# Optimization experiments

Measured on AMD Instinct MI355X. Metric: run time of the kernel, lower is better.

## Reference

```python
import jax, jax.numpy as jnp
import numpy as np

D_MODEL = 512
N_HEADS = 8
HEAD_DIM = D_MODEL // N_HEADS  # 64
N_LAYERS = 2
D_FF = 4 * D_MODEL
B, L, INPUT_DIM = 4, 1024, 32
SAMPLE_K = 35  # min(factor*ceil(ln L), L) with factor=5, L=1024
N_CLASSES = 10


def _layernorm(x, g, b, eps=1e-5):
    m = x.mean(-1, keepdims=True)
    v = ((x - m) ** 2).mean(-1, keepdims=True)
    return (x - m) / jnp.sqrt(v + eps) * g + b


def _pos_encoding(length, d):
    pos = np.arange(length, dtype=np.float32)[:, None]
    div = np.exp(np.arange(0, d, 2, dtype=np.float32) * (-np.log(10000.0) / d))
    pe = np.zeros((length, d), np.float32)
    pe[:, 0::2] = np.sin(pos * div)
    pe[:, 1::2] = np.cos(pos * div)
    return jnp.asarray(pe)


def _prob_attention(Q, K, V, idx_sample):
    # Q,K,V: (B,H,L,E); idx_sample: (L, sample_k) int
    b, h, l, e = Q.shape
    n_top = idx_sample.shape[-1]  # u == sample_k here since L_Q == L_K
    # K_sample gather: (B,H,L,sample_k,E)
    Ks = K[:, :, idx_sample, :]
    QK_sample = jnp.einsum('bhie,bhije->bhij', Q, Ks)  # (B,H,L,sample_k)
    M = QK_sample.max(-1) - QK_sample.mean(-1)          # sparsity measure
    _, idx_top = jax.lax.top_k(M, n_top)                # (B,H,n_top)
    Qr = jnp.take_along_axis(Q, idx_top[..., None], axis=2)  # (B,H,n_top,E)
    scale = 1.0 / jnp.sqrt(jnp.float32(e))
    scores = jnp.einsum('bhue,bhse->bhus', Qr, K) * scale    # (B,H,n_top,L)
    attn = jax.nn.softmax(scores, axis=-1)
    ctx_top = jnp.einsum('bhus,bhse->bhue', attn, V)
    # initial context: mean of V (mask_flag=False)
    context = jnp.broadcast_to(V.mean(axis=2, keepdims=True), (b, h, l, e))
    bi = jnp.arange(b)[:, None, None]
    hi = jnp.arange(h)[None, :, None]
    context = context.at[bi, hi, idx_top].set(ctx_top)
    return context.transpose(0, 2, 1, 3)  # (B,L,H,E)


def _attn_layer(x, Wq_l, bq_l, Wk_l, bk_l, Wv_l, bv_l, Wo_l, bo_l, idx_l):
    b, l, _ = x.shape
    Q = (x @ Wq_l + bq_l).reshape(b, l, N_HEADS, HEAD_DIM).transpose(0, 2, 1, 3)
    K = (x @ Wk_l + bk_l).reshape(b, l, N_HEADS, HEAD_DIM).transpose(0, 2, 1, 3)
    V = (x @ Wv_l + bv_l).reshape(b, l, N_HEADS, HEAD_DIM).transpose(0, 2, 1, 3)
    ctx = _prob_attention(Q, K, V, idx_l)  # (B,L,H,E)
    return ctx.reshape(b, l, -1) @ Wo_l + bo_l


def reference(src, idx_sample, Wemb, bemb, Wq, bq, Wk, bk, Wv, bv, Wo, bo,
              g1, beta1, W1, bf1, W2, bf2, g2, beta2, gf, betaf, Wc, bc):
    x = src @ Wemb + bemb                       # (B,L,D)
    x = x + _pos_encoding(x.shape[1], D_MODEL)[None]
    for layer in range(N_LAYERS):
        new_x = _attn_layer(x, Wq[layer], bq[layer], Wk[layer], bk[layer],
                            Wv[layer], bv[layer], Wo[layer], bo[layer],
                            idx_sample[layer])
        x = x + new_x                           # dropout off (eval)
        x = _layernorm(x, g1[layer], beta1[layer])
        y = jax.nn.gelu(x @ W1[layer] + bf1[layer], approximate=False)
        y = y @ W2[layer] + bf2[layer]
        x = _layernorm(x + y, g2[layer], beta2[layer])
    x = _layernorm(x, gf, betaf)
    pooled = x.mean(axis=1)                     # AdaptiveAvgPool1d(1) over seq
    return pooled @ Wc + bc                     # (B, num_classes)


def setup_inputs():
    key = jax.random.key(0)
    ks = jax.random.split(key, 16)
    s = 0.02
    nrm = lambda k, shape: jax.random.normal(k, shape, dtype=jnp.float32) * s
    inp = {}
    inp['src'] = jax.random.normal(ks[0], (B, L, INPUT_DIM), dtype=jnp.float32)
    inp['idx_sample'] = jax.random.randint(ks[1], (N_LAYERS, L, SAMPLE_K), 0, L)
    inp['Wemb'] = nrm(ks[2], (INPUT_DIM, D_MODEL))
    inp['bemb'] = jnp.zeros((D_MODEL,), jnp.float32)
    inp['Wq'] = nrm(ks[3], (N_LAYERS, D_MODEL, D_MODEL))
    inp['bq'] = jnp.zeros((N_LAYERS, D_MODEL), jnp.float32)
    inp['Wk'] = nrm(ks[4], (N_LAYERS, D_MODEL, D_MODEL))
    inp['bk'] = jnp.zeros((N_LAYERS, D_MODEL), jnp.float32)
    inp['Wv'] = nrm(ks[5], (N_LAYERS, D_MODEL, D_MODEL))
    inp['bv'] = jnp.zeros((N_LAYERS, D_MODEL), jnp.float32)
    inp['Wo'] = nrm(ks[6], (N_LAYERS, D_MODEL, D_MODEL))
    inp['bo'] = jnp.zeros((N_LAYERS, D_MODEL), jnp.float32)
    inp['g1'] = jnp.ones((N_LAYERS, D_MODEL), jnp.float32)
    inp['beta1'] = jnp.zeros((N_LAYERS, D_MODEL), jnp.float32)
    inp['W1'] = nrm(ks[7], (N_LAYERS, D_MODEL, D_FF))
    inp['bf1'] = jnp.zeros((N_LAYERS, D_FF), jnp.float32)
    inp['W2'] = nrm(ks[8], (N_LAYERS, D_FF, D_MODEL))
    inp['bf2'] = jnp.zeros((N_LAYERS, D_MODEL), jnp.float32)
    inp['g2'] = jnp.ones((N_LAYERS, D_MODEL), jnp.float32)
    inp['beta2'] = jnp.zeros((N_LAYERS, D_MODEL), jnp.float32)
    inp['gf'] = jnp.ones((D_MODEL,), jnp.float32)
    inp['betaf'] = jnp.zeros((D_MODEL,), jnp.float32)
    inp['Wc'] = nrm(ks[9], (D_MODEL, N_CLASSES))
    inp['bc'] = jnp.zeros((N_CLASSES,), jnp.float32)
    return inp
```

## Files before the change

### kernel.cpp

```cpp
#include <hip/hip_runtime.h>
#include <hip/hip_bf16.h>
#include <math.h>

#define B_ 4
#define L_ 1024
#define DM 512
#define NH 8
#define HD 64
#define DFF 2048
#define KS 35
#define QS 1536
#define CH 128
#define NCH (L_/CH)
#define VSEG 16

typedef __attribute__((ext_vector_type(8))) short bf16x8;
typedef __attribute__((ext_vector_type(4))) float f32x4;

__device__ inline ushort f2b(float f){
  __hip_bfloat16 h = __float2bfloat16(f);
  return *reinterpret_cast<ushort*>(&h);
}
__device__ inline float b2f(ushort u){
  union { unsigned int i; float f; } x; x.i = ((unsigned int)u) << 16; return x.f;
}
__device__ inline float gelu_exact(float x){
  return 0.5f*x*(1.0f+erff(x*0.7071067811865476f));
}

#define GLOAD16(g, l) __builtin_amdgcn_global_load_lds( \
    (const __attribute__((address_space(1))) void*)(g), \
    (__attribute__((address_space(3))) void*)(l), 16, 0, 0)

__global__ __launch_bounds__(256) void wconv_kernel(const float* __restrict__ W,
    ushort* __restrict__ Wt, int K, int N, size_t sStride, size_t dStride)
{
  W  += (size_t)blockIdx.z * sStride;
  Wt += (size_t)blockIdx.z * dStride;
  __shared__ float tile[32][33];
  int n0 = blockIdx.x*32, k0 = blockIdx.y*32;
  int tx = threadIdx.x & 31, ty = threadIdx.x >> 5;
  #pragma unroll
  for (int i = ty; i < 32; i += 8) tile[i][tx] = W[(size_t)(k0+i)*N + n0+tx];
  __syncthreads();
  #pragma unroll
  for (int i = ty; i < 32; i += 8) Wt[(size_t)(n0+i)*K + k0+tx] = f2b(tile[tx][i]);
}

__global__ __launch_bounds__(256) void wconv_qkv_kernel(const float* __restrict__ Wq,
    const float* __restrict__ Wk, const float* __restrict__ Wv, ushort* __restrict__ Wt)
{
  int z = blockIdx.z, which = z >> 1, l = z & 1;
  const float* W = ((which == 0) ? Wq : (which == 1) ? Wk : Wv) + (size_t)l*DM*DM;
  ushort* dst = Wt + (size_t)l*QS*DM + (size_t)which*512*DM;
  __shared__ float tile[32][33];
  int n0 = blockIdx.x*32, k0 = blockIdx.y*32;
  int tx = threadIdx.x & 31, ty = threadIdx.x >> 5;
  #pragma unroll
  for (int i = ty; i < 32; i += 8) tile[i][tx] = W[(size_t)(k0+i)*DM + n0+tx];
  __syncthreads();
  #pragma unroll
  for (int i = ty; i < 32; i += 8) dst[(size_t)(n0+i)*DM + k0+tx] = f2b(tile[tx][i]);
}

__global__ __launch_bounds__(256) void bcat_kernel(const float* __restrict__ bq,
    const float* __restrict__ bk, const float* __restrict__ bv, float* __restrict__ bqkv)
{
  int i = blockIdx.x*256 + threadIdx.x;
  if (i >= 2*QS) return;
  int l = i / QS, j = i - l*QS;
  const float* src = (j < 512) ? bq : (j < 1024 ? bk : bv);
  bqkv[i] = src[l*DM + (j & 511)];
}

template<int BM, int BN, int MODE>
__global__ __launch_bounds__(256) void mfma_gemm(
    const ushort* __restrict__ A, const ushort* __restrict__ Bt,
    const float* __restrict__ bias, const float* __restrict__ R,
    float* __restrict__ Cf, ushort* __restrict__ Cb,
    int M, int N, int K)
{
  constexpr int MF = BM/32;
  constexpr int NF = BN/32;
  constexpr int AIT = BM*4/256;
  constexpr int BIT = BN*4/256;
  constexpr int LT = (AIT + BIT)*2;
  __shared__ __align__(16) ushort As[2][2][BM*32];
  __shared__ __align__(16) ushort Bs[2][2][BN*32];
  const int t = threadIdx.x, lane = t & 63, w = t >> 6, wr = w >> 1, wc = w & 1;

  const int gx = gridDim.x;
  const int nwg = gx * gridDim.y;
  const int bid = blockIdx.y*gx + blockIdx.x;
  const int swz = (bid & 7)*(nwg >> 3) + (bid >> 3);
  const int row0 = (swz / gx)*BM, col0 = (swz % gx)*BN;

  const ushort* aSrc[AIT]; int aDst[AIT];
  #pragma unroll
  for (int j = 0; j < AIT; j++) {
    int ch = j*256 + t, r = ch >> 2, cc = ch & 3, cs = cc ^ ((r >> 1) & 3);
    aSrc[j] = A + (size_t)(row0 + r)*K + cs*8;
    aDst[j] = ch*16;
  }
  const ushort* bSrc[BIT]; int bDst[BIT];
  #pragma unroll
  for (int j = 0; j < BIT; j++) {
    int ch = j*256 + t, r = ch >> 2, cc = ch & 3, cs = cc ^ ((r >> 1) & 3);
    bSrc[j] = Bt + (size_t)(col0 + r)*K + cs*8;
    bDst[j] = ch*16;
  }
  int aOff[MF], bOff[NF];
  #pragma unroll
  for (int m = 0; m < MF; m++) {
    int r = wr*(BM/2) + m*16 + (lane & 15);
    aOff[m] = r*64 + (((lane >> 4)*16) ^ (((r >> 1) & 3) << 4));
  }
  #pragma unroll
  for (int n = 0; n < NF; n++) {
    int r = wc*(BN/2) + n*16 + (lane & 15);
    bOff[n] = r*64 + (((lane >> 4)*16) ^ (((r >> 1) & 3) << 4));
  }
  f32x4 zero = {0.f, 0.f, 0.f, 0.f};
  f32x4 acc[MF][NF];
  #pragma unroll
  for (int m = 0; m < MF; m++)
    #pragma unroll
    for (int n = 0; n < NF; n++) acc[m][n] = zero;

#define STAGE_TILE(kt, buf) do { \
    _Pragma("unroll") \
    for (int j = 0; j < AIT; j++) GLOAD16(aSrc[j] + (kt),      (char*)As[buf][0] + aDst[j]); \
    _Pragma("unroll") \
    for (int j = 0; j < AIT; j++) GLOAD16(aSrc[j] + (kt) + 32, (char*)As[buf][1] + aDst[j]); \
    _Pragma("unroll") \
    for (int j = 0; j < BIT; j++) GLOAD16(bSrc[j] + (kt),      (char*)Bs[buf][0] + bDst[j]); \
    _Pragma("unroll") \
    for (int j = 0; j < BIT; j++) GLOAD16(bSrc[j] + (kt) + 32, (char*)Bs[buf][1] + bDst[j]); \
  } while (0)

  const int nk = K >> 6;
  STAGE_TILE(0, 0);
  STAGE_TILE(64, 1);

  for (int ki = 0; ki < nk; ki++) {
    const int cur = ki & 1;
    if (ki + 1 < nk) {
      if constexpr (LT == 8)      asm volatile("s_waitcnt vmcnt(8)" ::: "memory");
      else if constexpr (LT == 6) asm volatile("s_waitcnt vmcnt(6)" ::: "memory");
      else                        asm volatile("s_waitcnt vmcnt(4)" ::: "memory");
    } else {
      asm volatile("s_waitcnt vmcnt(0)" ::: "memory");
    }
    __builtin_amdgcn_sched_barrier(0);
    __builtin_amdgcn_s_barrier();
    #pragma unroll
    for (int s = 0; s < 2; s++) {
      bf16x8 af[MF], bfr[NF];
      #pragma unroll
      for (int m = 0; m < MF; m++) af[m] = *(const bf16x8*)((const char*)As[cur][s] + aOff[m]);
      #pragma unroll
      for (int n = 0; n < NF; n++) bfr[n] = *(const bf16x8*)((const char*)Bs[cur][s] + bOff[n]);
      #pragma unroll
      for (int m = 0; m < MF; m++)
        #pragma unroll
        for (int n = 0; n < NF; n++)
          acc[m][n] = __builtin_amdgcn_mfma_f32_16x16x32_bf16(af[m], bfr[n], acc[m][n], 0, 0, 0);
    }
    __builtin_amdgcn_s_barrier();
    if (ki + 2 < nk) STAGE_TILE((ki + 2) << 6, cur);
  }
#undef STAGE_TILE

  #pragma unroll
  for (int m = 0; m < MF; m++) {
    int rb = row0 + wr*(BM/2) + m*16 + ((lane >> 4) << 2);
    #pragma unroll
    for (int n = 0; n < NF; n++) {
      int c = col0 + wc*(BN/2) + n*16 + (lane & 15);
      float bv = bias[c];
      #pragma unroll
      for (int j = 0; j < 4; j++) {
        size_t idx = (size_t)(rb + j)*N + c;
        float v = acc[m][n][j] + bv;
        if (MODE == 1)      Cb[idx] = f2b(gelu_exact(v));
        else if (MODE == 2) Cf[idx] = v + R[idx];
        else if (MODE == 3) Cb[idx] = f2b(v);
        else                Cf[idx] = v;
      }
    }
  }
}

__global__ __launch_bounds__(512) void embed_kernel(const float* __restrict__ src,
    const float* __restrict__ Wemb, const float* __restrict__ bemb,
    ushort* __restrict__ Xt)
{
  int row = blockIdx.x, l = row & (L_-1), t = threadIdx.x;
  __shared__ float s_src[32];
  if (t < 32) s_src[t] = src[row*32 + t];
  __syncthreads();
  float acc = bemb[t];
  #pragma unroll
  for (int k = 0; k < 32; k++) acc += s_src[k]*Wemb[k*DM + t];
  int i2 = t & ~1;
  float freq = expf((float)i2 * (-9.210340371976184f/512.0f));
  float ang = (float)l * freq;
  acc += (t & 1) ? cosf(ang) : sinf(ang);
  Xt[(size_t)row*DM + t] = f2b(acc);
}

__global__ __launch_bounds__(64) void qksample_kernel(const ushort* __restrict__ QKVb,
    const int* __restrict__ idx_s, float* __restrict__ Msc)
{
  int gid = blockIdx.x;
  int i = gid & (L_-1), h = (gid >> 10) & 7, b = gid >> 13;
  int t = threadIdx.x;
  int j4 = t >> 2, e4 = t & 3;
  const ushort* Qrow = QKVb + ((size_t)(b*L_ + i))*QS + h*HD + e4*16;
  bf16x8 qa = *(const bf16x8*)(Qrow);
  bf16x8 qb = *(const bf16x8*)(Qrow + 8);
  float q[16];
  #pragma unroll
  for (int x = 0; x < 8; x++) { q[x] = b2f((ushort)qa[x]); q[8+x] = b2f((ushort)qb[x]); }
  const ushort* Kbase = QKVb + 512 + h*HD + (size_t)b*L_*QS + e4*16;
  const int* idq = idx_s + i*KS;
  float mx = -3.4e38f, sm = 0.f;
  #pragma unroll
  for (int p = 0; p < 3; p++) {
    int j = p*16 + j4;
    int jc = (j < KS) ? j : 0;
    int s = idq[jc];
    const ushort* Kr = Kbase + (size_t)s*QS;
    bf16x8 ka = *(const bf16x8*)(Kr);
    bf16x8 kb = *(const bf16x8*)(Kr + 8);
    float d = 0.f;
    #pragma unroll
    for (int x = 0; x < 8; x++) d += q[x]   * b2f((ushort)ka[x]);
    #pragma unroll
    for (int x = 0; x < 8; x++) d += q[8+x] * b2f((ushort)kb[x]);
    d += __shfl_xor(d, 1);
    d += __shfl_xor(d, 2);
    if (j < KS && e4 == 0) { mx = fmaxf(mx, d); sm += d; }
  }
  #pragma unroll
  for (int off = 4; off < 64; off <<= 1) {
    mx = fmaxf(mx, __shfl_xor(mx, off));
    sm += __shfl_xor(sm, off);
  }
  if (t == 0) Msc[gid] = mx - sm*(1.0f/KS);
}

__global__ __launch_bounds__(64) void topk_kernel(const float* __restrict__ Msc, int* __restrict__ idx_top)
{
  int bh = blockIdx.x, t = threadIdx.x;
  float v[16];
  #pragma unroll
  for (int r = 0; r < 16; r++) v[r] = Msc[(size_t)bh*L_ + r*64 + t];
  for (int sel = 0; sel < KS; sel++) {
    float bv = -3.4e38f; int br = 0;
    #pragma unroll
    for (int r = 0; r < 16; r++) {
      bool gt = v[r] > bv;
      bv = gt ? v[r] : bv;
      br = gt ? r : br;
    }
    int bi = br*64 + t;
    #pragma unroll
    for (int off = 32; off; off >>= 1) {
      float ov = __shfl_xor(bv, off); int oi = __shfl_xor(bi, off);
      if (ov > bv || (ov == bv && oi < bi)) { bv = ov; bi = oi; }
    }
    if (t == 0) idx_top[bh*KS + sel] = bi;
    if ((bi & 63) == t) v[bi >> 6] = -3.4e38f;
  }
}

__global__ __launch_bounds__(64) void vmean_part_kernel(const ushort* __restrict__ QKVb,
    float* __restrict__ VmeanP)
{
  int gid = blockIdx.x;
  int seg = gid & (VSEG-1), bh = gid >> 4;
  int h = bh & 7, b = bh >> 3;
  int e = threadIdx.x;
  const ushort* Vb = QKVb + 1024 + h*HD + ((size_t)(b*L_ + seg*(L_/VSEG)))*QS;
  float s = 0.f;
  for (int l0 = 0; l0 < L_/VSEG; l0 += 8) {
    float vv[8];
    #pragma unroll
    for (int j = 0; j < 8; j++) vv[j] = b2f(Vb[(size_t)(l0+j)*QS + e]);
    #pragma unroll
    for (int j = 0; j < 8; j++) s += vv[j];
  }
  VmeanP[gid*HD + e] = s;
}

__global__ __launch_bounds__(64) void vmean_merge_kernel(const float* __restrict__ VmeanP,
    float* __restrict__ Vmean)
{
  int bh = blockIdx.x, e = threadIdx.x;
  float s = 0.f;
  #pragma unroll
  for (int seg = 0; seg < VSEG; seg++) s += VmeanP[(bh*VSEG + seg)*HD + e];
  Vmean[bh*HD + e] = s * (1.f/L_);
}

__global__ __launch_bounds__(512) void ctxfill_kernel(const float* __restrict__ Vmean, ushort* __restrict__ CTXb)
{
  int row = blockIdx.x, b = row >> 10, t = threadIdx.x;
  CTXb[(size_t)row*DM + t] = f2b(Vmean[b*DM + t]);
}

__global__ __launch_bounds__(256) void attn_part_kernel(const ushort* __restrict__ QKVb,
    const int* __restrict__ idx_top,
    float* __restrict__ Pacc, float* __restrict__ Pm, float* __restrict__ Pl)
{
  int gid = blockIdx.x;
  int q = gid & 3, c = (gid >> 2) & 7, bh = gid >> 5;
  int h = bh & 7, b = bh >> 3;
  int chunk = bh*NCH + c;
  int u0 = q*9;
  int NU = (q == 3) ? 8 : 9;
  int t = threadIdx.x;
  __shared__ float qs[9][68];
  __shared__ float sc[9][132];
  __shared__ float sm[9], sl[9];

  for (int idx = t; idx < NU*64; idx += 256) {
    int ul = idx >> 6, e = idx & 63;
    int qi = idx_top[bh*KS + u0 + ul];
    qs[ul][e] = b2f(QKVb[((size_t)(b*L_ + qi))*QS + h*HD + e]) * 0.125f;
  }
  __syncthreads();

  {
    int k = t & 127, par = t >> 7;
    const ushort* Kr = QKVb + ((size_t)(b*L_ + c*CH + k))*QS + 512 + h*HD;
    bf16x8 kreg[8];
    #pragma unroll
    for (int i8 = 0; i8 < 8; i8++) kreg[i8] = *(const bf16x8*)(Kr + i8*8);
    for (int ul = par; ul < NU; ul += 2) {
      float d = 0.f;
      #pragma unroll
      for (int i8 = 0; i8 < 8; i8++) {
        bf16x8 kv = kreg[i8];
        float4 qa = *(const float4*)&qs[ul][i8*8];
        float4 qb = *(const float4*)&qs[ul][i8*8 + 4];
        d += qa.x*b2f((ushort)kv[0]) + qa.y*b2f((ushort)kv[1])
           + qa.z*b2f((ushort)kv[2]) + qa.w*b2f((ushort)kv[3]);
        d += qb.x*b2f((ushort)kv[4]) + qb.y*b2f((ushort)kv[5])
           + qb.z*b2f((ushort)kv[6]) + qb.w*b2f((ushort)kv[7]);
      }
      sc[ul][k] = d;
    }
  }
  __syncthreads();

  {
    int ul = t >> 2, sub = t & 3;
    if (ul < NU) {
      float m = -3.4e38f;
      for (int i = sub; i < 128; i += 4) m = fmaxf(m, sc[ul][i]);
      m = fmaxf(m, __shfl_xor(m, 1));
      m = fmaxf(m, __shfl_xor(m, 2));
      float l = 0.f;
      for (int i = sub; i < 128; i += 4) {
        float ev = expf(sc[ul][i] - m);
        sc[ul][i] = ev;
        l += ev;
      }
      l += __shfl_xor(l, 1);
      l += __shfl_xor(l, 2);
      if (sub == 0) { sm[ul] = m; sl[ul] = l; }
    }
  }
  __syncthreads();

  {
    int e = t & 63, ug = t >> 6;
    const ushort* Vb = QKVb + 1024 + h*HD + ((size_t)(b*L_ + c*CH))*QS;
    float acc[3] = {0.f, 0.f, 0.f};
    for (int kb0 = 0; kb0 < CH; kb0 += 8) {
      float vv[8];
      #pragma unroll
      for (int j = 0; j < 8; j++) vv[j] = b2f(Vb[(size_t)(kb0 + j)*QS + e]);
      #pragma unroll
      for (int j = 0; j < 8; j++) {
        #pragma unroll
        for (int iu = 0; iu < 3; iu++) {
          int ul = ug + iu*4;
          if (ul < NU) acc[iu] += sc[ul][kb0 + j] * vv[j];
        }
      }
    }
    #pragma unroll
    for (int iu = 0; iu < 3; iu++) {
      int ul = ug + iu*4;
      if (ul < NU) Pacc[((size_t)chunk*35 + u0 + ul)*64 + e] = acc[iu];
    }
  }
  if (t < NU) { Pm[chunk*35 + u0 + t] = sm[t]; Pl[chunk*35 + u0 + t] = sl[t]; }
}

__global__ __launch_bounds__(256) void attn_merge_kernel(const float* __restrict__ Pacc,
    const float* __restrict__ Pm, const float* __restrict__ Pl,
    const int* __restrict__ idx_top, ushort* __restrict__ CTXb)
{
  int bh = blockIdx.x;
  int h = bh & 7, b = bh >> 3;
  int t = threadIdx.x;
  __shared__ float m8[NCH*35], l8[NCH*35];
  for (int i = t; i < NCH*35; i += 256) {
    int c = i / 35, u = i - c*35;
    m8[c*35 + u] = Pm[((size_t)bh*NCH + c)*35 + u];
    l8[c*35 + u] = Pl[((size_t)bh*NCH + c)*35 + u];
  }
  __syncthreads();
  int e = t & 63, ug = t >> 6;
  #pragma unroll
  for (int iu = 0; iu < 9; iu++) {
    int u = ug + iu*4;
    if (u >= 35) break;
    float M = -3.4e38f;
    #pragma unroll
    for (int c = 0; c < NCH; c++) M = fmaxf(M, m8[c*35 + u]);
    float Ltot = 0.f, o = 0.f;
    #pragma unroll
    for (int c = 0; c < NCH; c++) {
      float w = expf(m8[c*35 + u] - M);
      Ltot += w * l8[c*35 + u];
      o += w * Pacc[(((size_t)bh*NCH + c)*35 + u)*64 + e];
    }
    int qi = idx_top[bh*KS + u];
    CTXb[((size_t)(b*L_ + qi))*DM + h*HD + e] = f2b(o / Ltot);
  }
}

__global__ __launch_bounds__(512) void ln_kernel(const ushort* __restrict__ Xin,
    const ushort* __restrict__ AddB, const float* __restrict__ g, const float* __restrict__ beta,
    ushort* __restrict__ Xout)
{
  int row = blockIdx.x, t = threadIdx.x;
  __shared__ float red[16];
  size_t idx = (size_t)row*DM + t;
  float v = b2f(Xin[idx]);
  if (AddB) v += b2f(AddB[idx]);
  float s = v;
  #pragma unroll
  for (int off = 32; off; off >>= 1) s += __shfl_xor(s, off);
  if ((t & 63) == 0) red[t >> 6] = s;
  __syncthreads();
  float mean = 0.f;
  #pragma unroll
  for (int k = 0; k < 8; k++) mean += red[k];
  mean *= (1.f/DM);
  float d = v - mean, q = d*d;
  #pragma unroll
  for (int off = 32; off; off >>= 1) q += __shfl_xor(q, off);
  if ((t & 63) == 0) red[8 + (t >> 6)] = q;
  __syncthreads();
  float var = 0.f;
  #pragma unroll
  for (int k = 0; k < 8; k++) var += red[8 + k];
  var *= (1.f/DM);
  float r = d / sqrtf(var + 1e-5f) * g[t] + beta[t];
  Xout[idx] = f2b(r);
}

__global__ __launch_bounds__(512) void poolp_kernel(const ushort* __restrict__ Xt, float* __restrict__ pooledP)
{
  int p = blockIdx.x;
  int t = threadIdx.x;
  int b = p >> 3, seg = p & 7;
  float s = 0.f;
  const ushort* base = Xt + ((size_t)b*L_ + seg*128)*DM + t;
  for (int l = 0; l < 128; l++) s += b2f(base[(size_t)l*DM]);
  pooledP[p*DM + t] = s;
}

__global__ __launch_bounds__(64) void cls_kernel(const float* __restrict__ pooledP,
    const float* __restrict__ Wc, const float* __restrict__ bc, float* __restrict__ out)
{
  int o = blockIdx.x;
  int b = o/10, c = o%10, t = threadIdx.x;
  float s = 0.f;
  for (int d = t; d < DM; d += 64) {
    float p = 0.f;
    #pragma unroll
    for (int seg = 0; seg < 8; seg++) p += pooledP[(b*8 + seg)*DM + d];
    s += p * (1.f/L_) * Wc[d*10 + c];
  }
  #pragma unroll
  for (int off = 32; off; off >>= 1) s += __shfl_xor(s, off);
  if (t == 0) out[o] = bc[c] + s;
}

extern "C" void kernel_launch(void* const* d_in, const int* in_sizes, int n_in,
                              void* d_out, int out_size, void* d_ws, size_t ws_size,
                              hipStream_t stream)
{
  const float* src   = (const float*)d_in[0];
  const int*   idxs  = (const int*)d_in[1];
  const float* Wemb  = (const float*)d_in[2];
  const float* bemb  = (const float*)d_in[3];
  const float* Wq    = (const float*)d_in[4];
  const float* bq    = (const float*)d_in[5];
  const float* Wk    = (const float*)d_in[6];
  const float* bk    = (const float*)d_in[7];
  const float* Wv    = (const float*)d_in[8];
  const float* bv    = (const float*)d_in[9];
  const float* Wo    = (const float*)d_in[10];
  const float* bo    = (const float*)d_in[11];
  const float* g1    = (const float*)d_in[12];
  const float* beta1 = (const float*)d_in[13];
  const float* W1    = (const float*)d_in[14];
  const float* bf1   = (const float*)d_in[15];
  const float* W2    = (const float*)d_in[16];
  const float* bf2   = (const float*)d_in[17];
  const float* g2    = (const float*)d_in[18];
  const float* beta2 = (const float*)d_in[19];
  const float* gf    = (const float*)d_in[20];
  const float* betaf = (const float*)d_in[21];
  const float* Wc    = (const float*)d_in[22];
  const float* bc    = (const float*)d_in[23];
  float* out = (float*)d_out;

  float* wsf = (float*)d_ws;
  float*  Pacc  = wsf;
  float*  VmeanP = wsf + 573440;
  ushort* Xt    = (ushort*)(wsf + 2097152);
  ushort* CTXb  = (ushort*)(wsf + 3145728);
  ushort* QKVb  = (ushort*)(wsf + 4194304);
  ushort* Ob    = (ushort*)(wsf + 7340032);
  ushort* H     = (ushort*)(wsf + 4194304);
  ushort* Yb    = (ushort*)(wsf + 8388608);
  ushort* Wqkvt = (ushort*)(wsf + 10485760);
  ushort* Wot   = (ushort*)(wsf + 11272192);
  ushort* W1t   = (ushort*)(wsf + 11534336);
  ushort* W2t   = (ushort*)(wsf + 12582912);
  float*  bqkv  = wsf + 13631488;
  float*  Msc   = wsf + 13634560;
  float*  Pm    = wsf + 13634560;
  float*  Pl    = wsf + 13634560 + 8960;
  float*  Vmean = wsf + 13667328;
  float*  pooledP = wsf + 13669376;
  int*    idx_top = (int*)(wsf + 13685760);

  wconv_qkv_kernel<<<dim3(DM/32, DM/32, 6), 256, 0, stream>>>(Wq, Wk, Wv, Wqkvt);
  wconv_kernel<<<dim3(DM/32, DM/32, 2), 256, 0, stream>>>(Wo, Wot, DM, DM, (size_t)DM*DM, (size_t)DM*DM);
  wconv_kernel<<<dim3(DFF/32, DM/32, 2), 256, 0, stream>>>(W1, W1t, DM, DFF, (size_t)DM*DFF, (size_t)DFF*DM);
  wconv_kernel<<<dim3(DM/32, DFF/32, 2), 256, 0, stream>>>(W2, W2t, DFF, DM, (size_t)DFF*DM, (size_t)DM*DFF);
  bcat_kernel<<<12, 256, 0, stream>>>(bq, bk, bv, bqkv);

  const int M = B_ * L_;
  embed_kernel<<<M, 512, 0, stream>>>(src, Wemb, bemb, Xt);

  for (int l = 0; l < 2; l++) {
    const size_t vo = (size_t)l*DM;
    mfma_gemm<128,128,3><<<dim3(QS/128, M/128), 256, 0, stream>>>(
        Xt, Wqkvt + (size_t)l*QS*DM, bqkv + (size_t)l*QS, nullptr, nullptr, QKVb, M, QS, DM);
    qksample_kernel<<<B_*NH*L_, 64, 0, stream>>>(QKVb, idxs + (size_t)l*L_*KS, Msc);
    topk_kernel<<<B_*NH, 64, 0, stream>>>(Msc, idx_top);
    vmean_part_kernel<<<B_*NH*VSEG, 64, 0, stream>>>(QKVb, VmeanP);
    vmean_merge_kernel<<<B_*NH, 64, 0, stream>>>(VmeanP, Vmean);
    ctxfill_kernel<<<M, 512, 0, stream>>>(Vmean, CTXb);
    attn_part_kernel<<<B_*NH*NCH*4, 256, 0, stream>>>(QKVb, idx_top, Pacc, Pm, Pl);
    attn_merge_kernel<<<B_*NH, 256, 0, stream>>>(Pacc, Pm, Pl, idx_top, CTXb);
    mfma_gemm<64,64,3><<<dim3(DM/64, M/64), 256, 0, stream>>>(
        CTXb, Wot + (size_t)l*DM*DM, bo + vo, nullptr, nullptr, Ob, M, DM, DM);
    ln_kernel<<<M, 512, 0, stream>>>(Xt, Ob, g1 + vo, beta1 + vo, Xt);
    mfma_gemm<128,128,1><<<dim3(DFF/128, M/128), 256, 0, stream>>>(
        Xt, W1t + (size_t)l*DFF*DM, bf1 + (size_t)l*DFF, nullptr, nullptr, H, M, DFF, DM);
    mfma_gemm<64,64,3><<<dim3(DM/64, M/64), 256, 0, stream>>>(
        H, W2t + (size_t)l*DM*DFF, bf2 + vo, nullptr, nullptr, Yb, M, DM, DFF);
    ln_kernel<<<M, 512, 0, stream>>>(Xt, Yb, g2 + vo, beta2 + vo, Xt);
  }
  ln_kernel<<<M, 512, 0, stream>>>(Xt, nullptr, gf, betaf, Xt);
  poolp_kernel<<<B_*8, 512, 0, stream>>>(Xt, pooledP);
  cls_kernel<<<40, 64, 0, stream>>>(pooledP, Wc, bc, out);
}
```

Before: 392.7 us.

## Replace output projection GEMM with mean-based base GEMV plus sparse per-row deltas

Because the context is the per-(batch,head) V mean everywhere except the top-k selected rows, the output projection is rewritten as a per-batch GEMV of Vmean through Wo plus sparse corrections for the selected rows. A mask/entry map built from idx_top tells each row which heads need a delta times the Wo slice. This drops the full M×512×512 MFMA GEMM, the context fill, and the Wo bf16 conversion, at the cost of an fp32 scalar projection for the few selected rows and some atomics. Numerics change slightly because Wo is applied in fp32 instead of bf16.

Result: slower. 446.9 us (+13.8%).

```diff
diff --git a/kernel.cpp b/kernel.cpp
--- a/kernel.cpp
+++ b/kernel.cpp
@@ -276,12 +276,13 @@
 }
 
 __global__ __launch_bounds__(64) void vmean_part_kernel(const ushort* __restrict__ QKVb,
-    float* __restrict__ VmeanP)
+    float* __restrict__ VmeanP, int* __restrict__ mask)
 {
   int gid = blockIdx.x;
+  int e = threadIdx.x;
+  if (gid < 64) mask[gid*64 + e] = 0;
   int seg = gid & (VSEG-1), bh = gid >> 4;
   int h = bh & 7, b = bh >> 3;
-  int e = threadIdx.x;
   const ushort* Vb = QKVb + 1024 + h*HD + ((size_t)(b*L_ + seg*(L_/VSEG)))*QS;
   float s = 0.f;
   for (int l0 = 0; l0 < L_/VSEG; l0 += 8) {
@@ -304,10 +305,86 @@
   Vmean[bh*HD + e] = s * (1.f/L_);
 }
 
-__global__ __launch_bounds__(512) void ctxfill_kernel(const float* __restrict__ Vmean, ushort* __restrict__ CTXb)
-{
-  int row = blockIdx.x, b = row >> 10, t = threadIdx.x;
-  CTXb[(size_t)row*DM + t] = f2b(Vmean[b*DM + t]);
+__global__ __launch_bounds__(256) void build_map_kernel(const int* __restrict__ idx_top,
+    int* __restrict__ mask, int* __restrict__ ent)
+{
+  int idx = blockIdx.x*256 + threadIdx.x;
+  if (idx >= B_*NH*KS) return;
+  int bh = idx / KS;
+  int b = bh >> 3, h = bh & 7;
+  int qi = idx_top[idx];
+  int row = b*L_ + qi;
+  atomicOr(&mask[row], 1 << h);
+  ent[row*8 + h] = idx;
+}
+
+__global__ __launch_bounds__(512) void gemv_base_kernel(const float* __restrict__ Vmean,
+    const float* __restrict__ Wo_l, const float* __restrict__ bo_l, float* __restrict__ base)
+{
+  int b = blockIdx.x, c = threadIdx.x;
+  __shared__ float vm[512];
+  vm[c] = Vmean[b*DM + c];
+  __syncthreads();
+  float acc = bo_l[c];
+  for (int e0 = 0; e0 < DM; e0 += 8) {
+    float wv[8];
+    #pragma unroll
+    for (int j = 0; j < 8; j++) wv[j] = Wo_l[(size_t)(e0+j)*DM + c];
+    #pragma unroll
+    for (int j = 0; j < 8; j++) acc += vm[e0+j]*wv[j];
+  }
+  base[b*DM + c] = acc;
+}
+
+__global__ __launch_bounds__(256) void attn_merge_delta_kernel(const float* __restrict__ Pacc,
+    const float* __restrict__ Pm, const float* __restrict__ Pl,
+    const float* __restrict__ Vmean, float* __restrict__ D)
+{
+  int bh = blockIdx.x;
+  int t = threadIdx.x;
+  __shared__ float m8[NCH*35], l8[NCH*35];
+  for (int i = t; i < NCH*35; i += 256) {
+    int c = i / 35, u = i - c*35;
+    m8[c*35 + u] = Pm[((size_t)bh*NCH + c)*35 + u];
+    l8[c*35 + u] = Pl[((size_t)bh*NCH + c)*35 + u];
+  }
+  __syncthreads();
+  int e = t & 63, ug = t >> 6;
+  float vm = Vmean[bh*HD + e];
+  #pragma unroll
+  for (int iu = 0; iu < 9; iu++) {
+    int u = ug + iu*4;
+    if (u >= 35) break;
+    float M = -3.4e38f;
+    #pragma unroll
+    for (int c = 0; c < NCH; c++) M = fmaxf(M, m8[c*35 + u]);
+    float Ltot = 0.f, o = 0.f;
+    #pragma unroll
+    for (int c = 0; c < NCH; c++) {
+      float w = expf(m8[c*35 + u] - M);
+      Ltot += w * l8[c*35 + u];
+      o += w * Pacc[(((size_t)bh*NCH + c)*35 + u)*64 + e];
+    }
+    D[((size_t)bh*KS + u)*64 + e] = o / Ltot - vm;
+  }
+}
+
+__global__ __launch_bounds__(512) void ob_fill_kernel(const float* __restrict__ base,
+    const float* __restrict__ D, const int* __restrict__ mask, const int* __restrict__ ent,
+    const float* __restrict__ Wo_l, ushort* __restrict__ Ob)
+{
+  int l = blockIdx.x, b = l >> 10, c = threadIdx.x;
+  float acc = base[b*DM + c];
+  int mk = mask[l];
+  while (mk) {
+    int h = __ffs(mk) - 1; mk &= mk - 1;
+    int enc = ent[l*8 + h];
+    const float* dp = D + (size_t)enc*64;
+    const float* wr = Wo_l + (size_t)(h*64)*DM + c;
+    #pragma unroll 8
+    for (int e = 0; e < 64; e++) acc += dp[e] * wr[(size_t)e*DM];
+  }
+  Ob[(size_t)l*DM + c] = f2b(acc);
 }
 
 __global__ __launch_bounds__(256) void attn_part_kernel(const ushort* __restrict__ QKVb,
@@ -399,40 +476,6 @@
     }
   }
   if (t < NU) { Pm[chunk*35 + u0 + t] = sm[t]; Pl[chunk*35 + u0 + t] = sl[t]; }
-}
-
-__global__ __launch_bounds__(256) void attn_merge_kernel(const float* __restrict__ Pacc,
-    const float* __restrict__ Pm, const float* __restrict__ Pl,
-    const int* __restrict__ idx_top, ushort* __restrict__ CTXb)
-{
-  int bh = blockIdx.x;
-  int h = bh & 7, b = bh >> 3;
-  int t = threadIdx.x;
-  __shared__ float m8[NCH*35], l8[NCH*35];
-  for (int i = t; i < NCH*35; i += 256) {
-    int c = i / 35, u = i - c*35;
-    m8[c*35 + u] = Pm[((size_t)bh*NCH + c)*35 + u];
-    l8[c*35 + u] = Pl[((size_t)bh*NCH + c)*35 + u];
-  }
-  __syncthreads();
-  int e = t & 63, ug = t >> 6;
-  #pragma unroll
-  for (int iu = 0; iu < 9; iu++) {
-    int u = ug + iu*4;
-    if (u >= 35) break;
-    float M = -3.4e38f;
-    #pragma unroll
-    for (int c = 0; c < NCH; c++) M = fmaxf(M, m8[c*35 + u]);
-    float Ltot = 0.f, o = 0.f;
-    #pragma unroll
-    for (int c = 0; c < NCH; c++) {
-      float w = expf(m8[c*35 + u] - M);
-      Ltot += w * l8[c*35 + u];
-      o += w * Pacc[(((size_t)bh*NCH + c)*35 + u)*64 + e];
-    }
-    int qi = idx_top[bh*KS + u];
-    CTXb[((size_t)(b*L_ + qi))*DM + h*HD + e] = f2b(o / Ltot);
-  }
 }
 
 __global__ __launch_bounds__(512) void ln_kernel(const ushort* __restrict__ Xin,
@@ -527,14 +570,16 @@
   float* wsf = (float*)d_ws;
   float*  Pacc  = wsf;
   float*  VmeanP = wsf + 573440;
+  float*  D     = wsf + 606208;
+  float*  base  = wsf + 677888;
+  int*    mask  = (int*)(wsf + 679936);
+  int*    ent   = (int*)(wsf + 684032);
   ushort* Xt    = (ushort*)(wsf + 2097152);
-  ushort* CTXb  = (ushort*)(wsf + 3145728);
   ushort* QKVb  = (ushort*)(wsf + 4194304);
   ushort* Ob    = (ushort*)(wsf + 7340032);
   ushort* H     = (ushort*)(wsf + 4194304);
   ushort* Yb    = (ushort*)(wsf + 8388608);
   ushort* Wqkvt = (ushort*)(wsf + 10485760);
-  ushort* Wot   = (ushort*)(wsf + 11272192);
   ushort* W1t   = (ushort*)(wsf + 11534336);
   ushort* W2t   = (ushort*)(wsf + 12582912);
   float*  bqkv  = wsf + 13631488;
@@ -546,7 +591,6 @@
   int*    idx_top = (int*)(wsf + 13685760);
 
   wconv_qkv_kernel<<<dim3(DM/32, DM/32, 6), 256, 0, stream>>>(Wq, Wk, Wv, Wqkvt);
-  wconv_kernel<<<dim3(DM/32, DM/32, 2), 256, 0, stream>>>(Wo, Wot, DM, DM, (size_t)DM*DM, (size_t)DM*DM);
   wconv_kernel<<<dim3(DFF/32, DM/32, 2), 256, 0, stream>>>(W1, W1t, DM, DFF, (size_t)DM*DFF, (size_t)DFF*DM);
   wconv_kernel<<<dim3(DM/32, DFF/32, 2), 256, 0, stream>>>(W2, W2t, DFF, DM, (size_t)DFF*DM, (size_t)DM*DFF);
   bcat_kernel<<<12, 256, 0, stream>>>(bq, bk, bv, bqkv);
@@ -556,17 +600,18 @@
 
   for (int l = 0; l < 2; l++) {
     const size_t vo = (size_t)l*DM;
+    const float* Wo_l = Wo + (size_t)l*DM*DM;
     mfma_gemm<128,128,3><<<dim3(QS/128, M/128), 256, 0, stream>>>(
         Xt, Wqkvt + (size_t)l*QS*DM, bqkv + (size_t)l*QS, nullptr, nullptr, QKVb, M, QS, DM);
     qksample_kernel<<<B_*NH*L_, 64, 0, stream>>>(QKVb, idxs + (size_t)l*L_*KS, Msc);
     topk_kernel<<<B_*NH, 64, 0, stream>>>(Msc, idx_top);
-    vmean_part_kernel<<<B_*NH*VSEG, 64, 0, stream>>>(QKVb, VmeanP);
+    vmean_part_kernel<<<B_*NH*VSEG, 64, 0, stream>>>(QKVb, VmeanP, mask);
     vmean_merge_kernel<<<B_*NH, 64, 0, stream>>>(VmeanP, Vmean);
-    ctxfill_kernel<<<M, 512, 0, stream>>>(Vmean, CTXb);
+    build_map_kernel<<<(B_*NH*KS + 255)/256, 256, 0, stream>>>(idx_top, mask, ent);
+    gemv_base_kernel<<<B_, 512, 0, stream>>>(Vmean, Wo_l, bo + vo, base);
     attn_part_kernel<<<B_*NH*NCH*4, 256, 0, stream>>>(QKVb, idx_top, Pacc, Pm, Pl);
-    attn_merge_kernel<<<B_*NH, 256, 0, stream>>>(Pacc, Pm, Pl, idx_top, CTXb);
-    mfma_gemm<64,64,3><<<dim3(DM/64, M/64), 256, 0, stream>>>(
-        CTXb, Wot + (size_t)l*DM*DM, bo + vo, nullptr, nullptr, Ob, M, DM, DM);
+    attn_merge_delta_kernel<<<B_*NH, 256, 0, stream>>>(Pacc, Pm, Pl, Vmean, D);
+    ob_fill_kernel<<<M, 512, 0, stream>>>(base, D, mask, ent, Wo_l, Ob);
     ln_kernel<<<M, 512, 0, stream>>>(Xt, Ob, g1 + vo, beta1 + vo, Xt);
     mfma_gemm<128,128,1><<<dim3(DFF/128, M/128), 256, 0, stream>>>(
         Xt, W1t + (size_t)l*DFF*DM, bf1 + (size_t)l*DFF, nullptr, nullptr, H, M, DFF, DM);
```
